# Kernel tuning notes

Hardware: AMD Instinct MI355X
Metric: run time of the kernel (lower is better)

Reference implementation:

```python
import jax, jax.numpy as jnp
import numpy as np

EPS = 1e-5

def _conv(x, w, b, dil, pad, groups):
    y = jax.lax.conv_general_dilated(
        x, w, window_strides=(1, 1), padding=[(pad, pad), (pad, pad)],
        rhs_dilation=(dil, dil), dimension_numbers=('NCHW', 'OIHW', 'NCHW'),
        feature_group_count=groups)
    return y + b[None, :, None, None]

def setup_inputs() -> dict:
    key = jax.random.key(0)
    ks = jax.random.split(key, 12)
    B, C, H, W = 16, 128, 128, 128
    half = C // 2  # 64
    x = jax.random.normal(ks[0], (B, C, H, W), dtype=jnp.float32)
    # depthwise 3x3 (groups=half) + pointwise 1x1
    dw_w = jax.random.normal(ks[1], (half, 1, 3, 3), dtype=jnp.float32) * 0.1
    dw_b = jax.random.normal(ks[2], (half,), dtype=jnp.float32) * 0.1
    pw_w = jax.random.normal(ks[3], (half, half, 1, 1), dtype=jnp.float32) * (1.0 / np.sqrt(half))
    pw_b = jax.random.normal(ks[4], (half,), dtype=jnp.float32) * 0.1
    # four 1->1 channel 3x3 convs with dilations 1..4 (weights shared across blocks)
    mcc_w = jax.random.normal(ks[5], (4, 1, 1, 3, 3), dtype=jnp.float32) * 0.2
    mcc_b = jax.random.normal(ks[6], (4,), dtype=jnp.float32) * 0.1
    gamma = jnp.ones((C,), dtype=jnp.float32)
    beta = jnp.zeros((C,), dtype=jnp.float32)
    return {"x": x, "dw_w": dw_w, "dw_b": dw_b, "pw_w": pw_w, "pw_b": pw_b,
            "mcc_w": mcc_w, "mcc_b": mcc_b, "gamma": gamma, "beta": beta}

def reference(x, dw_w, dw_b, pw_w, pw_b, mcc_w, mcc_b, gamma, beta):
    B, C, H, W = x.shape
    half = C // 2
    nblk = half // 4
    # split_channel: even channels -> x1, odd channels -> x2
    x1 = x[:, 0::2]
    x2 = x[:, 1::2]
    # branch 1: depthwise 3x3 then pointwise 1x1
    x1 = _conv(x1, dw_w, dw_b, dil=1, pad=1, groups=half)
    x1 = _conv(x1, pw_w, pw_b, dil=1, pad=0, groups=1)
    # branch 2: channel i of x2 goes through dilated conv (i mod 4); vectorize by
    # gathering channels j::4 and running one depthwise conv per dilation.
    ys = []
    for j in range(4):
        d = j + 1
        xj = x2[:, j::4]                       # [B, nblk, H, W]
        wj = jnp.tile(mcc_w[j], (nblk, 1, 1, 1))  # [nblk,1,3,3] shared kernel
        bj = jnp.tile(mcc_b[j], (nblk,))
        ys.append(_conv(xj, wj, bj, dil=d, pad=d, groups=nblk))
    # interleave back: channel 4*b+j <- ys[j][:, b]
    mcc = jnp.stack(ys, axis=2).reshape(B, half, H, W)
    fusion = jnp.concatenate([x1, mcc], axis=1)  # [B, C, H, W]
    # BatchNorm2d (training mode: batch statistics, biased variance) + ReLU
    mean = jnp.mean(fusion, axis=(0, 2, 3), keepdims=True)
    var = jnp.var(fusion, axis=(0, 2, 3), keepdims=True)
    norm = (fusion - mean) * jax.lax.rsqrt(var + EPS)
    out = norm * gamma[None, :, None, None] + beta[None, :, None, None]
    return jax.nn.relu(out)
```

## Files before the change

kernel.cpp:

```cpp
#include <hip/hip_runtime.h>
#include <hip/hip_bf16.h>

#define Bn 16
#define Cn 128
#define Hn 128
#define Wn 128
#define HWn (Hn*Wn)
#define CHWn (Cn*HWn)
#define HALF 64
#define NTOT (Bn*HWn)
#define NSLOT 32

#define DT_P 76
#define WL_P 76
#define CB_P 136

typedef __attribute__((ext_vector_type(8))) short short8;
typedef __attribute__((ext_vector_type(4))) float floatx4;

__device__ __forceinline__ float4 fma4(float s, float4 v, float4 a) {
  a.x = fmaf(s, v.x, a.x); a.y = fmaf(s, v.y, a.y);
  a.z = fmaf(s, v.z, a.z); a.w = fmaf(s, v.w, a.w);
  return a;
}
__device__ __forceinline__ unsigned short f2bf(float f) {
  union { __hip_bfloat16 h; unsigned short u; } cv;
  cv.h = __float2bfloat16(f); return cv.u;
}
__device__ __forceinline__ float bf2f(unsigned short u) {
  union { unsigned short u; __hip_bfloat16 h; } cv; cv.u = u;
  return __bfloat162float(cv.h);
}
__device__ __forceinline__ unsigned pk2f(float a, float b) {
  return (unsigned)f2bf(a) | ((unsigned)f2bf(b) << 16);
}
__device__ __forceinline__ short8 ld_frag(const unsigned short* p) {
  union { uint2 u[2]; short8 s; } cv;
  cv.u[0] = *(const uint2*)p;
  cv.u[1] = *(const uint2*)(p + 4);
  return cv.s;
}

__device__ __forceinline__ float4 row3(float4 acc, float4 B, float wa, float wb,
                                       float wc, int lane31) {
  float xl = __shfl_up(B.w, 1);
  float xr = __shfl_down(B.x, 1);
  if (lane31 == 0)  xl = 0.f;
  if (lane31 == 31) xr = 0.f;
  float4 L = make_float4(xl, B.x, B.y, B.z);
  float4 R = make_float4(B.y, B.z, B.w, xr);
  acc = fma4(wa, L, acc);
  acc = fma4(wb, B, acc);
  acc = fma4(wc, R, acc);
  return acc;
}

template<bool BF16>
__device__ __forceinline__ void dwpw_body(
    const int item, const int t, unsigned char* __restrict__ smem,
    const float* __restrict__ x, const float* __restrict__ pw_w,
    const float* __restrict__ dw_w, const float* __restrict__ dw_b,
    const float* __restrict__ pw_b, float* __restrict__ outf,
    __hip_bfloat16* __restrict__ outh, float* __restrict__ stats)
{
  unsigned short* DtCb = (unsigned short*)smem;
  unsigned short* Wl   = (unsigned short*)(smem + 128*DT_P*2);
  float* dww  = (float*)(smem + 128*DT_P*2 + 64*WL_P*2);
  float* sred = dww + 640;

  const int band = item & 7;
  const int ri   = item >> 3;
  const int h = band*16 + (ri & 15);
  const int b = ri >> 4;

  for (int i = t; i < 1024; i += 256) {
    int c = i >> 4, k4 = (i & 15) << 2;
    float4 w = ((const float4*)pw_w)[i];
    union { unsigned short us[4]; uint2 u; } cv;
    cv.us[0] = f2bf(w.x); cv.us[1] = f2bf(w.y);
    cv.us[2] = f2bf(w.z); cv.us[3] = f2bf(w.w);
    *(uint2*)&Wl[c*WL_P + k4] = cv.u;
  }
  for (int i = t; i < 576; i += 256) {
    int k = i / 9, j = i - k*9;
    dww[j*64 + k] = dw_w[i];
  }
  if (t < 64)  dww[576 + t] = dw_b[t];
  if (t < 128) sred[t] = 0.f;
  __syncthreads();

  {
    const int lane31 = t & 31;
    const int px4 = lane31 << 2;
    const int k0 = t >> 5;
    const float* xb = x + (size_t)b*CHWn + (size_t)h*Wn + px4;
    const bool hasU = (h > 0), hasD = (h < Hn-1);
    const float4 z4 = make_float4(0.f,0.f,0.f,0.f);
    unsigned pkq[4][4];
    unsigned lo[4];
    #pragma unroll
    for (int i = 0; i < 8; ++i) {
      const int k = k0*8 + i;
      const float* xc = xb + (size_t)(2*k)*HWn;
      float4 r0 = hasU ? *(const float4*)(xc - Wn) : z4;
      float4 r1 = *(const float4*)xc;
      float4 r2 = hasD ? *(const float4*)(xc + Wn) : z4;
      float bk = dww[576 + k];
      float4 a = make_float4(bk, bk, bk, bk);
      a = row3(a, r0, dww[0*64+k], dww[1*64+k], dww[2*64+k], lane31);
      a = row3(a, r1, dww[3*64+k], dww[4*64+k], dww[5*64+k], lane31);
      a = row3(a, r2, dww[6*64+k], dww[7*64+k], dww[8*64+k], lane31);
      float av[4] = {a.x, a.y, a.z, a.w};
      if ((i & 1) == 0) {
        #pragma unroll
        for (int j = 0; j < 4; ++j) lo[j] = f2bf(av[j]);
      } else {
        #pragma unroll
        for (int j = 0; j < 4; ++j)
          pkq[j][i>>1] = lo[j] | ((unsigned)f2bf(av[j]) << 16);
      }
    }
    #pragma unroll
    for (int j = 0; j < 4; ++j) {
      unsigned short* p = &DtCb[(px4+j)*DT_P + k0*8];
      uint2 w0; w0.x = pkq[j][0]; w0.y = pkq[j][1];
      uint2 w1; w1.x = pkq[j][2]; w1.y = pkq[j][3];
      *(uint2*)p       = w0;
      *(uint2*)(p + 4) = w1;
    }
  }
  __syncthreads();

  const int lane = t & 63;
  const int wv   = t >> 6;
  const int q4   = lane >> 4;
  const int n16  = lane & 15;

  short8 Af[4][2], Bf[2][2];
  #pragma unroll
  for (int ct = 0; ct < 4; ++ct)
    #pragma unroll
    for (int kc = 0; kc < 2; ++kc)
      Af[ct][kc] = ld_frag(&Wl[(ct*16 + n16)*WL_P + kc*32 + q4*8]);
  #pragma unroll
  for (int nt = 0; nt < 2; ++nt)
    #pragma unroll
    for (int kc = 0; kc < 2; ++kc)
      Bf[nt][kc] = ld_frag(&DtCb[(wv*32 + nt*16 + n16)*DT_P + kc*32 + q4*8]);

  floatx4 C[4][2];
  #pragma unroll
  for (int ct = 0; ct < 4; ++ct) {
    float4 bs = *(const float4*)&pw_b[ct*16 + q4*4];
    floatx4 ini = {bs.x, bs.y, bs.z, bs.w};
    C[ct][0] = ini; C[ct][1] = ini;
  }
  #pragma unroll
  for (int kc = 0; kc < 2; ++kc)
    #pragma unroll
    for (int ct = 0; ct < 4; ++ct)
      #pragma unroll
      for (int nt = 0; nt < 2; ++nt)
        C[ct][nt] = __builtin_amdgcn_mfma_f32_16x16x32_bf16(
            Af[ct][kc], Bf[nt][kc], C[ct][nt], 0, 0, 0);

  __syncthreads();

  #pragma unroll
  for (int ct = 0; ct < 4; ++ct) {
    float S[4], Q[4];
    #pragma unroll
    for (int r = 0; r < 4; ++r) {
      float a = C[ct][0][r], c2 = C[ct][1][r];
      S[r] = a + c2;
      Q[r] = a*a + c2*c2;
    }
    #pragma unroll
    for (int off = 1; off < 16; off <<= 1)
      #pragma unroll
      for (int r = 0; r < 4; ++r) {
        S[r] += __shfl_xor(S[r], off);
        Q[r] += __shfl_xor(Q[r], off);
      }
    if (n16 == 0) {
      #pragma unroll
      for (int r = 0; r < 4; ++r) {
        int c = ct*16 + q4*4 + r;
        atomicAdd(&sred[c], S[r]);
        atomicAdd(&sred[64 + c], Q[r]);
      }
    }
  }

  const size_t ob = (size_t)b*CHWn + (size_t)h*Wn;
  if (BF16) {
    #pragma unroll
    for (int ct = 0; ct < 4; ++ct)
      #pragma unroll
      for (int nt = 0; nt < 2; ++nt)
        #pragma unroll
        for (int r = 0; r < 4; ++r) {
          int c  = ct*16 + q4*4 + r;
          int px = wv*32 + nt*16 + n16;
          DtCb[c*CB_P + px] = f2bf(C[ct][nt][r]);
        }
  } else {
    #pragma unroll
    for (int ct = 0; ct < 4; ++ct)
      #pragma unroll
      for (int nt = 0; nt < 2; ++nt)
        #pragma unroll
        for (int r = 0; r < 4; ++r) {
          int c  = ct*16 + q4*4 + r;
          int px = wv*32 + nt*16 + n16;
          outf[ob + (size_t)c*HWn + px] = C[ct][nt][r];
        }
  }
  __syncthreads();

  if (BF16) {
    for (int i = t; i < 1024; i += 256) {
      int c = i >> 4, p8 = (i & 15) << 3;
      uint4 v = *(const uint4*)&DtCb[c*CB_P + p8];
      *(uint4*)(outh + ob + (size_t)c*HWn + p8) = v;
    }
  }
  float* sg = stats + (item & (NSLOT-1))*256;
  if (t < 64)       atomicAdd(&sg[t], sred[t]);
  else if (t < 128) atomicAdd(&sg[64 + t], sred[t]);
}

template<int D> __device__ __forceinline__ float4 shiftL(float4 A, float4 B) {
  if (D == 1) return make_float4(A.w, B.x, B.y, B.z);
  if (D == 2) return make_float4(A.z, A.w, B.x, B.y);
  if (D == 3) return make_float4(A.y, A.z, A.w, B.x);
  return A;
}
template<int D> __device__ __forceinline__ float4 shiftR(float4 B, float4 C) {
  if (D == 1) return make_float4(B.y, B.z, B.w, C.x);
  if (D == 2) return make_float4(B.z, B.w, C.x, C.y);
  if (D == 3) return make_float4(B.w, C.x, C.y, C.z);
  return C;
}

template<bool BF16, int D>
__device__ __forceinline__ void mcc_compute(
    const float* __restrict__ xc, const float* __restrict__ wj, float bj,
    float* __restrict__ outf, __hip_bfloat16* __restrict__ outh,
    float* lds, int t, int h0, float& s, float& q)
{
  const int R = 16 + 2*D;
  for (int idx = t; idx < R*32; idx += 256) {
    int r = idx >> 5, p4 = (idx & 31) << 2;
    int gr = h0 - D + r;
    float4 v = make_float4(0.f,0.f,0.f,0.f);
    if (gr >= 0 && gr < Hn) v = *(const float4*)(xc + gr*Wn + p4);
    *(float4*)&lds[r*128 + p4] = v;
  }
  __syncthreads();
  const int px4 = (t & 31) << 2;
  const int rl  = t >> 5;
  s = 0.f; q = 0.f;
  #pragma unroll
  for (int rr = 0; rr < 2; ++rr) {
    const int row = rl + rr*8;
    float4 acc = make_float4(bj, bj, bj, bj);
    #pragma unroll
    for (int dr = 0; dr < 3; ++dr) {
      const float* lrow = &lds[(row + dr*D)*128];
      float4 B4 = *(const float4*)(lrow + px4);
      float4 A4 = make_float4(0.f,0.f,0.f,0.f);
      float4 C4 = make_float4(0.f,0.f,0.f,0.f);
      if (px4 > 0)   A4 = *(const float4*)(lrow + px4 - 4);
      if (px4 < 124) C4 = *(const float4*)(lrow + px4 + 4);
      acc = fma4(wj[dr*3+0], shiftL<D>(A4, B4), acc);
      acc = fma4(wj[dr*3+1], B4, acc);
      acc = fma4(wj[dr*3+2], shiftR<D>(B4, C4), acc);
    }
    if (BF16) {
      uint2 pk; pk.x = pk2f(acc.x, acc.y); pk.y = pk2f(acc.z, acc.w);
      *(uint2*)(outh + (size_t)(h0+row)*Wn + px4) = pk;
    } else {
      *(float4*)(outf + (size_t)(h0+row)*Wn + px4) = acc;
    }
    s += acc.x + acc.y + acc.z + acc.w;
    q += acc.x*acc.x + acc.y*acc.y + acc.z*acc.z + acc.w*acc.w;
  }
}

template<bool BF16>
__device__ __forceinline__ void mcc_body(
    const int mi, const int t, unsigned char* __restrict__ smem,
    const float* __restrict__ x, const float* __restrict__ mcc_w,
    const float* __restrict__ mcc_b, float* __restrict__ outf,
    __hip_bfloat16* __restrict__ outh, float* __restrict__ stats)
{
  float* lds = (float*)smem;
  float* red = lds + 24*128;

  const int hb = mi & 7;
  const int m  = (mi >> 3) & 63;
  const int b  = mi >> 9;
  const int j  = m & 3;
  const int h0 = hb << 4;

  const float* xc = x + (size_t)b*CHWn + (size_t)(2*m+1)*HWn;
  const size_t oo = (size_t)b*CHWn + (size_t)(HALF+m)*HWn;
  float* of = BF16 ? nullptr : outf + oo;
  __hip_bfloat16* oh = BF16 ? outh + oo : nullptr;
  const float* wj = mcc_w + j*9;
  const float bj = mcc_b[j];

  float s = 0.f, q = 0.f;
  switch (j) {
    case 0:  mcc_compute<BF16,1>(xc, wj, bj, of, oh, lds, t, h0, s, q); break;
    case 1:  mcc_compute<BF16,2>(xc, wj, bj, of, oh, lds, t, h0, s, q); break;
    case 2:  mcc_compute<BF16,3>(xc, wj, bj, of, oh, lds, t, h0, s, q); break;
    default: mcc_compute<BF16,4>(xc, wj, bj, of, oh, lds, t, h0, s, q); break;
  }

  #pragma unroll
  for (int off = 32; off > 0; off >>= 1) {
    s += __shfl_down(s, off);
    q += __shfl_down(q, off);
  }
  const int wvi = t >> 6;
  if ((t & 63) == 0) { red[wvi] = s; red[4+wvi] = q; }
  __syncthreads();
  if (t == 0) {
    float* sg = stats + (mi & (NSLOT-1))*256;
    atomicAdd(&sg[HALF + m],       red[0]+red[1]+red[2]+red[3]);
    atomicAdd(&sg[128 + HALF + m], red[4]+red[5]+red[6]+red[7]);
  }
}

template<bool BF16>
__global__ __launch_bounds__(256, 2) void fused_kernel(
    const float* __restrict__ x, const float* __restrict__ pw_w,
    const float* __restrict__ dw_w, const float* __restrict__ dw_b,
    const float* __restrict__ pw_b, const float* __restrict__ mcc_w,
    const float* __restrict__ mcc_b, float* __restrict__ outf,
    __hip_bfloat16* __restrict__ outh, float* __restrict__ stats)
{
  __shared__ __align__(16) unsigned char smem[32256];
  const int bid = blockIdx.x;
  const int t = threadIdx.x;
  const int qt = bid / 5;
  if (bid - qt*5 == 0)
    dwpw_body<BF16>(qt, t, smem, x, pw_w, dw_w, dw_b, pw_b, outf, outh, stats);
  else
    mcc_body<BF16>(bid - qt - 1, t, smem, x, mcc_w, mcc_b, outf, outh, stats);
}

__device__ __forceinline__ void replica_scale(const float* __restrict__ statsr,
                                              int c, int t, float* ssc)
{
  if (t < 64) {
    const int rl = t & 31;
    const int idx = (t < 32) ? c : (128 + c);
    float v = statsr[rl*256 + idx];
    #pragma unroll
    for (int off = 1; off < 32; off <<= 1) v += __shfl_xor(v, off);
    float S = __shfl(v, 0);
    float Q = __shfl(v, 32);
    if (t == 0) {
      const float n = (float)NTOT;
      float mean = S / n;
      float var  = Q / n - mean*mean;
      float sc = ssc[2] * rsqrtf(var + 1e-5f) * sqrtf(var + 1e-5f);
      (void)sc;
      float scale = ssc[2];
      (void)scale;
      ssc[0] = 0.f;
      float g = ssc[2], be = ssc[3];
      float s2 = g / sqrtf(var + 1e-5f);
      ssc[0] = s2;
      ssc[1] = be - mean * s2;
    }
  }
  __syncthreads();
}

__global__ __launch_bounds__(256) void norm_bf_kernel(
    const unsigned short* __restrict__ inh, float* __restrict__ out,
    const float* __restrict__ statsr, const float* __restrict__ gamma,
    const float* __restrict__ beta)
{
  __shared__ float ssc[4];
  const int blk = blockIdx.x;
  const int plane = blk >> 1;
  const int half = blk & 1;
  const int c = plane & 127;
  const int t = threadIdx.x;
  if (t == 0) { ssc[2] = gamma[c]; ssc[3] = beta[c]; }
  __syncthreads();
  replica_scale(statsr, c, t, ssc);
  const float sc = ssc[0], sh = ssc[1];

  const uint4* in = (const uint4*)(inh + (size_t)plane*HWn) + half*1024;
  float* op = out + (size_t)plane*HWn + half*8192;
  #pragma unroll
  for (int i = 0; i < 4; ++i) {
    int idx = t + i*256;
    uint4 p = in[idx];
    float4 a, bq;
    a.x = fmaxf(fmaf(bf2f(p.x & 0xffff), sc, sh), 0.f);
    a.y = fmaxf(fmaf(bf2f(p.x >> 16),    sc, sh), 0.f);
    a.z = fmaxf(fmaf(bf2f(p.y & 0xffff), sc, sh), 0.f);
    a.w = fmaxf(fmaf(bf2f(p.y >> 16),    sc, sh), 0.f);
    bq.x = fmaxf(fmaf(bf2f(p.z & 0xffff), sc, sh), 0.f);
    bq.y = fmaxf(fmaf(bf2f(p.z >> 16),    sc, sh), 0.f);
    bq.z = fmaxf(fmaf(bf2f(p.w & 0xffff), sc, sh), 0.f);
    bq.w = fmaxf(fmaf(bf2f(p.w >> 16),    sc, sh), 0.f);
    *(float4*)(op + idx*8)     = a;
    *(float4*)(op + idx*8 + 4) = bq;
  }
}

__global__ __launch_bounds__(256) void norm_f32_kernel(float* __restrict__ out,
    const float* __restrict__ statsr, const float* __restrict__ gamma,
    const float* __restrict__ beta)
{
  __shared__ float ssc[4];
  const int blk = blockIdx.x;
  const int plane = blk >> 1;
  const int half = blk & 1;
  const int c = plane & 127;
  const int t = threadIdx.x;
  if (t == 0) { ssc[2] = gamma[c]; ssc[3] = beta[c]; }
  __syncthreads();
  replica_scale(statsr, c, t, ssc);
  const float sc = ssc[0], sh = ssc[1];

  float* op = out + (size_t)plane*HWn + half*8192;
  #pragma unroll
  for (int i = 0; i < 8; ++i) {
    int idx = t + i*256;
    float4 v = ((const float4*)op)[idx];
    v.x = fmaxf(fmaf(v.x, sc, sh), 0.f);
    v.y = fmaxf(fmaf(v.y, sc, sh), 0.f);
    v.z = fmaxf(fmaf(v.z, sc, sh), 0.f);
    v.w = fmaxf(fmaf(v.w, sc, sh), 0.f);
    ((float4*)op)[idx] = v;
  }
}

extern "C" void kernel_launch(void* const* d_in, const int* in_sizes, int n_in,
                              void* d_out, int out_size, void* d_ws, size_t ws_size,
                              hipStream_t stream)
{
  (void)in_sizes; (void)n_in; (void)out_size;
  const float* x     = (const float*)d_in[0];
  const float* dw_w  = (const float*)d_in[1];
  const float* dw_b  = (const float*)d_in[2];
  const float* pw_w  = (const float*)d_in[3];
  const float* pw_b  = (const float*)d_in[4];
  const float* mcc_w = (const float*)d_in[5];
  const float* mcc_b = (const float*)d_in[6];
  const float* gamma = (const float*)d_in[7];
  const float* beta  = (const float*)d_in[8];
  float* out   = (float*)d_out;
  float* stats = (float*)d_ws;
  __hip_bfloat16* bf = (__hip_bfloat16*)((char*)d_ws + NSLOT*256*4);
  const size_t need = (size_t)NSLOT*256*4 + (size_t)Bn*CHWn*2;
  const bool useBF = ws_size >= need;

  hipMemsetAsync(d_ws, 0, NSLOT*256*4, stream);
  const int nblk = 2048 + Bn*HALF*(Hn/16);
  if (useBF) {
    fused_kernel<true><<<nblk, 256, 0, stream>>>(x, pw_w, dw_w, dw_b, pw_b,
                                                 mcc_w, mcc_b, nullptr, bf, stats);
    norm_bf_kernel<<<Bn*Cn*2, 256, 0, stream>>>((const unsigned short*)bf, out,
                                                stats, gamma, beta);
  } else {
    fused_kernel<false><<<nblk, 256, 0, stream>>>(x, pw_w, dw_w, dw_b, pw_b,
                                                  mcc_w, mcc_b, out, nullptr, stats);
    norm_f32_kernel<<<Bn*Cn*2, 256, 0, stream>>>(out, stats, gamma, beta);
  }
}
```

Baseline: 342.7 us.

## Merge conv, BN-stat finalize and normalize into one cooperative persistent kernel

Replaces the fused conv kernel plus separate normalize kernel with a persistent cooperative mega-kernel. It loops over work items, grid-syncs, computes per-channel scale/shift once, grid-syncs again, then normalizes with nontemporal stores. It also shrinks LDS by loading the pointwise weights straight from global into registers, which targets higher occupancy (launch bounds 256,5). The aim is to remove launch gaps and redundant per-block stat reductions, at the cost of grid-sync overhead and a fixed persistent grid size.

Result: slower. 776.5 us (+126.6%).

```diff
diff --git a/kernel.cpp b/kernel.cpp
--- a/kernel.cpp
+++ b/kernel.cpp
@@ -1,5 +1,8 @@
 #include <hip/hip_runtime.h>
 #include <hip/hip_bf16.h>
+#include <hip/hip_cooperative_groups.h>
+
+namespace cg = cooperative_groups;
 
 #define Bn 16
 #define Cn 128
@@ -10,13 +13,15 @@
 #define HALF 64
 #define NTOT (Bn*HWn)
 #define NSLOT 32
+#define NITEM 10240
 
 #define DT_P 76
-#define WL_P 76
 #define CB_P 136
+#define SMEM_BYTES 22528
 
 typedef __attribute__((ext_vector_type(8))) short short8;
 typedef __attribute__((ext_vector_type(4))) float floatx4;
+typedef float __attribute__((ext_vector_type(4))) f32x4;
 
 __device__ __forceinline__ float4 fma4(float s, float4 v, float4 a) {
   a.x = fmaf(s, v.x, a.x); a.y = fmaf(s, v.y, a.y);
@@ -39,6 +44,10 @@
   cv.u[0] = *(const uint2*)p;
   cv.u[1] = *(const uint2*)(p + 4);
   return cv.s;
+}
+__device__ __forceinline__ void st_nt4(float* p, float4 v) {
+  f32x4 w = {v.x, v.y, v.z, v.w};
+  __builtin_nontemporal_store(w, (f32x4*)p);
 }
 
 __device__ __forceinline__ float4 row3(float4 acc, float4 B, float wa, float wb,
@@ -64,8 +73,7 @@
     __hip_bfloat16* __restrict__ outh, float* __restrict__ stats)
 {
   unsigned short* DtCb = (unsigned short*)smem;
-  unsigned short* Wl   = (unsigned short*)(smem + 128*DT_P*2);
-  float* dww  = (float*)(smem + 128*DT_P*2 + 64*WL_P*2);
+  float* dww  = (float*)(smem + 128*DT_P*2);
   float* sred = dww + 640;
 
   const int band = item & 7;
@@ -73,14 +81,6 @@
   const int h = band*16 + (ri & 15);
   const int b = ri >> 4;
 
-  for (int i = t; i < 1024; i += 256) {
-    int c = i >> 4, k4 = (i & 15) << 2;
-    float4 w = ((const float4*)pw_w)[i];
-    union { unsigned short us[4]; uint2 u; } cv;
-    cv.us[0] = f2bf(w.x); cv.us[1] = f2bf(w.y);
-    cv.us[2] = f2bf(w.z); cv.us[3] = f2bf(w.w);
-    *(uint2*)&Wl[c*WL_P + k4] = cv.u;
-  }
   for (int i = t; i < 576; i += 256) {
     int k = i / 9, j = i - k*9;
     dww[j*64 + k] = dw_w[i];
@@ -96,7 +96,6 @@
     const float* xb = x + (size_t)b*CHWn + (size_t)h*Wn + px4;
     const bool hasU = (h > 0), hasD = (h < Hn-1);
     const float4 z4 = make_float4(0.f,0.f,0.f,0.f);
-    unsigned pkq[4][4];
     unsigned lo[4];
     #pragma unroll
     for (int i = 0; i < 8; ++i) {
@@ -116,17 +115,11 @@
         for (int j = 0; j < 4; ++j) lo[j] = f2bf(av[j]);
       } else {
         #pragma unroll
-        for (int j = 0; j < 4; ++j)
-          pkq[j][i>>1] = lo[j] | ((unsigned)f2bf(av[j]) << 16);
+        for (int j = 0; j < 4; ++j) {
+          unsigned pk = lo[j] | ((unsigned)f2bf(av[j]) << 16);
+          *(unsigned*)&DtCb[(px4+j)*DT_P + k0*8 + (i-1)] = pk;
+        }
       }
-    }
-    #pragma unroll
-    for (int j = 0; j < 4; ++j) {
-      unsigned short* p = &DtCb[(px4+j)*DT_P + k0*8];
-      uint2 w0; w0.x = pkq[j][0]; w0.y = pkq[j][1];
-      uint2 w1; w1.x = pkq[j][2]; w1.y = pkq[j][3];
-      *(uint2*)p       = w0;
-      *(uint2*)(p + 4) = w1;
     }
   }
   __syncthreads();
@@ -140,8 +133,15 @@
   #pragma unroll
   for (int ct = 0; ct < 4; ++ct)
     #pragma unroll
-    for (int kc = 0; kc < 2; ++kc)
-      Af[ct][kc] = ld_frag(&Wl[(ct*16 + n16)*WL_P + kc*32 + q4*8]);
+    for (int kc = 0; kc < 2; ++kc) {
+      const float* wp = pw_w + (ct*16 + n16)*64 + kc*32 + q4*8;
+      float4 w0 = *(const float4*)wp;
+      float4 w1 = *(const float4*)(wp + 4);
+      union { unsigned u[4]; short8 s; } cv;
+      cv.u[0] = pk2f(w0.x, w0.y); cv.u[1] = pk2f(w0.z, w0.w);
+      cv.u[2] = pk2f(w1.x, w1.y); cv.u[3] = pk2f(w1.z, w1.w);
+      Af[ct][kc] = cv.s;
+    }
   #pragma unroll
   for (int nt = 0; nt < 2; ++nt)
     #pragma unroll
@@ -225,6 +225,8 @@
       *(uint4*)(outh + ob + (size_t)c*HWn + p8) = v;
     }
   }
+  __syncthreads();
+
   float* sg = stats + (item & (NSLOT-1))*256;
   if (t < 64)       atomicAdd(&sg[t], sred[t]);
   else if (t < 128) atomicAdd(&sg[64 + t], sred[t]);
@@ -334,70 +336,16 @@
   }
 }
 
-template<bool BF16>
-__global__ __launch_bounds__(256, 2) void fused_kernel(
-    const float* __restrict__ x, const float* __restrict__ pw_w,
-    const float* __restrict__ dw_w, const float* __restrict__ dw_b,
-    const float* __restrict__ pw_b, const float* __restrict__ mcc_w,
-    const float* __restrict__ mcc_b, float* __restrict__ outf,
-    __hip_bfloat16* __restrict__ outh, float* __restrict__ stats)
-{
-  __shared__ __align__(16) unsigned char smem[32256];
-  const int bid = blockIdx.x;
-  const int t = threadIdx.x;
-  const int qt = bid / 5;
-  if (bid - qt*5 == 0)
-    dwpw_body<BF16>(qt, t, smem, x, pw_w, dw_w, dw_b, pw_b, outf, outh, stats);
-  else
-    mcc_body<BF16>(bid - qt - 1, t, smem, x, mcc_w, mcc_b, outf, outh, stats);
-}
-
-__device__ __forceinline__ void replica_scale(const float* __restrict__ statsr,
-                                              int c, int t, float* ssc)
-{
-  if (t < 64) {
-    const int rl = t & 31;
-    const int idx = (t < 32) ? c : (128 + c);
-    float v = statsr[rl*256 + idx];
-    #pragma unroll
-    for (int off = 1; off < 32; off <<= 1) v += __shfl_xor(v, off);
-    float S = __shfl(v, 0);
-    float Q = __shfl(v, 32);
-    if (t == 0) {
-      const float n = (float)NTOT;
-      float mean = S / n;
-      float var  = Q / n - mean*mean;
-      float sc = ssc[2] * rsqrtf(var + 1e-5f) * sqrtf(var + 1e-5f);
-      (void)sc;
-      float scale = ssc[2];
-      (void)scale;
-      ssc[0] = 0.f;
-      float g = ssc[2], be = ssc[3];
-      float s2 = g / sqrtf(var + 1e-5f);
-      ssc[0] = s2;
-      ssc[1] = be - mean * s2;
-    }
-  }
-  __syncthreads();
-}
-
-__global__ __launch_bounds__(256) void norm_bf_kernel(
-    const unsigned short* __restrict__ inh, float* __restrict__ out,
-    const float* __restrict__ statsr, const float* __restrict__ gamma,
-    const float* __restrict__ beta)
-{
-  __shared__ float ssc[4];
-  const int blk = blockIdx.x;
-  const int plane = blk >> 1;
-  const int half = blk & 1;
+__device__ __forceinline__ void norm_half_plane(
+    const unsigned short* __restrict__ bf, float* __restrict__ out,
+    const float* __restrict__ scsh, int hp, int t)
+{
+  const int plane = hp >> 1;
+  const int half  = hp & 1;
   const int c = plane & 127;
-  const int t = threadIdx.x;
-  if (t == 0) { ssc[2] = gamma[c]; ssc[3] = beta[c]; }
-  __syncthreads();
-  replica_scale(statsr, c, t, ssc);
-  const float sc = ssc[0], sh = ssc[1];
-
-  const uint4* in = (const uint4*)(inh + (size_t)plane*HWn) + half*1024;
+  const float sc = scsh[2*c], sh = scsh[2*c+1];
+
+  const uint4* in = (const uint4*)(bf + (size_t)plane*HWn) + half*1024;
   float* op = out + (size_t)plane*HWn + half*8192;
   #pragma unroll
   for (int i = 0; i < 4; ++i) {
@@ -412,30 +360,121 @@
     bq.y = fmaxf(fmaf(bf2f(p.z >> 16),    sc, sh), 0.f);
     bq.z = fmaxf(fmaf(bf2f(p.w & 0xffff), sc, sh), 0.f);
     bq.w = fmaxf(fmaf(bf2f(p.w >> 16),    sc, sh), 0.f);
-    *(float4*)(op + idx*8)     = a;
-    *(float4*)(op + idx*8 + 4) = bq;
-  }
+    st_nt4(op + idx*8,     a);
+    st_nt4(op + idx*8 + 4, bq);
+  }
+}
+
+__global__ __launch_bounds__(256, 5) void mega_kernel(
+    const float* __restrict__ x, const float* __restrict__ pw_w,
+    const float* __restrict__ dw_w, const float* __restrict__ dw_b,
+    const float* __restrict__ pw_b, const float* __restrict__ mcc_w,
+    const float* __restrict__ mcc_b, const float* __restrict__ gamma,
+    const float* __restrict__ beta, __hip_bfloat16* __restrict__ bf,
+    float* __restrict__ stats, float* __restrict__ scsh,
+    float* __restrict__ out)
+{
+  __shared__ __align__(16) unsigned char smem[SMEM_BYTES];
+  cg::grid_group gg = cg::this_grid();
+  const int t = threadIdx.x;
+  const int G = gridDim.x;
+
+  for (int item = blockIdx.x; item < NITEM; item += G) {
+    const int q = item / 5;
+    if (item - q*5 == 0)
+      dwpw_body<true>(q, t, smem, x, pw_w, dw_w, dw_b, pw_b,
+                      nullptr, bf, stats);
+    else
+      mcc_body<true>(item - q - 1, t, smem, x, mcc_w, mcc_b,
+                     nullptr, bf, stats);
+  }
+  __threadfence();
+  gg.sync();
+
+  for (int c = blockIdx.x; c < Cn; c += G) {
+    if (t < 64) {
+      int idx = (t < 32) ? c : (128 + c);
+      float v = stats[(t & 31)*256 + idx];
+      #pragma unroll
+      for (int off = 1; off < 32; off <<= 1) v += __shfl_xor(v, off);
+      float S = __shfl(v, 0);
+      float Q = __shfl(v, 32);
+      if (t == 0) {
+        const float n = (float)NTOT;
+        float mean = S / n;
+        float var  = Q / n - mean*mean;
+        float sc = gamma[c] / sqrtf(var + 1e-5f);
+        scsh[2*c]   = sc;
+        scsh[2*c+1] = beta[c] - mean*sc;
+      }
+    }
+  }
+  __threadfence();
+  gg.sync();
+
+  for (int hp = blockIdx.x; hp < Bn*Cn*2; hp += G)
+    norm_half_plane((const unsigned short*)bf, out, scsh, hp, t);
+}
+
+template<bool BF16>
+__global__ __launch_bounds__(256, 5) void fused_kernel(
+    const float* __restrict__ x, const float* __restrict__ pw_w,
+    const float* __restrict__ dw_w, const float* __restrict__ dw_b,
+    const float* __restrict__ pw_b, const float* __restrict__ mcc_w,
+    const float* __restrict__ mcc_b, float* __restrict__ outf,
+    __hip_bfloat16* __restrict__ outh, float* __restrict__ stats)
+{
+  __shared__ __align__(16) unsigned char smem[SMEM_BYTES];
+  const int bid = blockIdx.x;
+  const int t = threadIdx.x;
+  const int qt = bid / 5;
+  if (bid - qt*5 == 0)
+    dwpw_body<BF16>(qt, t, smem, x, pw_w, dw_w, dw_b, pw_b, outf, outh, stats);
+  else
+    mcc_body<BF16>(bid - qt - 1, t, smem, x, mcc_w, mcc_b, outf, outh, stats);
+}
+
+__global__ __launch_bounds__(64) void finalize_kernel(
+    const float* __restrict__ stats, const float* __restrict__ gamma,
+    const float* __restrict__ beta, float* __restrict__ scsh)
+{
+  const int c = blockIdx.x;
+  const int t = threadIdx.x;
+  int idx = (t < 32) ? c : (128 + c);
+  float v = stats[(t & 31)*256 + idx];
+  #pragma unroll
+  for (int off = 1; off < 32; off <<= 1) v += __shfl_xor(v, off);
+  float S = __shfl(v, 0);
+  float Q = __shfl(v, 32);
+  if (t == 0) {
+    const float n = (float)NTOT;
+    float mean = S / n;
+    float var  = Q / n - mean*mean;
+    float sc = gamma[c] / sqrtf(var + 1e-5f);
+    scsh[2*c]   = sc;
+    scsh[2*c+1] = beta[c] - mean*sc;
+  }
+}
+
+__global__ __launch_bounds__(256) void norm_bf_kernel(
+    const unsigned short* __restrict__ inh, float* __restrict__ out,
+    const float* __restrict__ scsh)
+{
+  norm_half_plane(inh, out, scsh, blockIdx.x, threadIdx.x);
 }
 
 __global__ __launch_bounds__(256) void norm_f32_kernel(float* __restrict__ out,
-    const float* __restrict__ statsr, const float* __restrict__ gamma,
-    const float* __restrict__ beta)
-{
-  __shared__ float ssc[4];
+    const float* __restrict__ scsh)
+{
   const int blk = blockIdx.x;
   const int plane = blk >> 1;
   const int half = blk & 1;
   const int c = plane & 127;
-  const int t = threadIdx.x;
-  if (t == 0) { ssc[2] = gamma[c]; ssc[3] = beta[c]; }
-  __syncthreads();
-  replica_scale(statsr, c, t, ssc);
-  const float sc = ssc[0], sh = ssc[1];
-
+  const float sc = scsh[2*c], sh = scsh[2*c+1];
   float* op = out + (size_t)plane*HWn + half*8192;
   #pragma unroll
   for (int i = 0; i < 8; ++i) {
-    int idx = t + i*256;
+    int idx = threadIdx.x + i*256;
     float4 v = ((const float4*)op)[idx];
     v.x = fmaxf(fmaf(v.x, sc, sh), 0.f);
     v.y = fmaxf(fmaf(v.y, sc, sh), 0.f);
@@ -461,20 +500,49 @@
   const float* beta  = (const float*)d_in[8];
   float* out   = (float*)d_out;
   float* stats = (float*)d_ws;
-  __hip_bfloat16* bf = (__hip_bfloat16*)((char*)d_ws + NSLOT*256*4);
-  const size_t need = (size_t)NSLOT*256*4 + (size_t)Bn*CHWn*2;
+  float* scsh  = (float*)((char*)d_ws + 32768);
+  __hip_bfloat16* bf = (__hip_bfloat16*)((char*)d_ws + 34816);
+  const size_t need = 34816 + (size_t)Bn*CHWn*2;
   const bool useBF = ws_size >= need;
 
-  hipMemsetAsync(d_ws, 0, NSLOT*256*4, stream);
-  const int nblk = 2048 + Bn*HALF*(Hn/16);
-  if (useBF) {
-    fused_kernel<true><<<nblk, 256, 0, stream>>>(x, pw_w, dw_w, dw_b, pw_b,
-                                                 mcc_w, mcc_b, nullptr, bf, stats);
-    norm_bf_kernel<<<Bn*Cn*2, 256, 0, stream>>>((const unsigned short*)bf, out,
-                                                stats, gamma, beta);
+  static int g_init = 0, g_coop = 0, g_grid = 0;
+  if (!g_init) {
+    int dev = 0; (void)hipGetDevice(&dev);
+    int sup = 0;
+    (void)hipDeviceGetAttribute(&sup, hipDeviceAttributeCooperativeLaunch, dev);
+    hipDeviceProp_t prop;
+    (void)hipGetDeviceProperties(&prop, dev);
+    int nb = 0;
+    (void)hipOccupancyMaxActiveBlocksPerMultiprocessor(&nb, mega_kernel, 256, 0);
+    long G = (long)nb * prop.multiProcessorCount;
+    G = (G / 40) * 40;
+    if (G > 1280) G = 1280;
+    g_grid = (int)G;
+    g_coop = (sup && G >= 40) ? 1 : 0;
+    g_init = 1;
+  }
+
+  hipMemsetAsync(d_ws, 0, 32768, stream);
+  if (useBF && g_coop) {
+    void* args[13];
+    args[0]  = (void*)&x;     args[1]  = (void*)&pw_w;
+    args[2]  = (void*)&dw_w;  args[3]  = (void*)&dw_b;
+    args[4]  = (void*)&pw_b;  args[5]  = (void*)&mcc_w;
+    args[6]  = (void*)&mcc_b; args[7]  = (void*)&gamma;
+    args[8]  = (void*)&beta;  args[9]  = (void*)&bf;
+    args[10] = (void*)&stats; args[11] = (void*)&scsh;
+    args[12] = (void*)&out;
+    (void)hipLaunchCooperativeKernel(mega_kernel, dim3(g_grid), dim3(256),
+                                     args, 0, stream);
+  } else if (useBF) {
+    fused_kernel<true><<<NITEM, 256, 0, stream>>>(x, pw_w, dw_w, dw_b, pw_b,
+                                                  mcc_w, mcc_b, nullptr, bf, stats);
+    finalize_kernel<<<Cn, 64, 0, stream>>>(stats, gamma, beta, scsh);
+    norm_bf_kernel<<<Bn*Cn*2, 256, 0, stream>>>((const unsigned short*)bf, out, scsh);
   } else {
-    fused_kernel<false><<<nblk, 256, 0, stream>>>(x, pw_w, dw_w, dw_b, pw_b,
-                                                  mcc_w, mcc_b, out, nullptr, stats);
-    norm_f32_kernel<<<Bn*Cn*2, 256, 0, stream>>>(out, stats, gamma, beta);
-  }
-}
+    fused_kernel<false><<<NITEM, 256, 0, stream>>>(x, pw_w, dw_w, dw_b, pw_b,
+                                                   mcc_w, mcc_b, out, nullptr, stats);
+    finalize_kernel<<<Cn, 64, 0, stream>>>(stats, gamma, beta, scsh);
+    norm_f32_kernel<<<Bn*Cn*2, 256, 0, stream>>>(out, scsh);
+  }
+}
```
